# Performance work log

Measured on AMD Instinct MI355X. Metric: run time of the kernel, lower is better.

## Reference

```python
import jax, jax.numpy as jnp
import numpy as np
from jax import lax

B, T, E, H = 256, 512, 256, 256

def setup_inputs() -> dict:
    key = jax.random.key(0)
    k1, k2, k3, k4, k5 = jax.random.split(key, 5)
    s_in = 1.0 / np.sqrt(E)
    s_h = 1.0 / np.sqrt(H)
    return {
        "x": jax.random.normal(k1, (B, T, E), dtype=jnp.float32),
        "Wx_w": jax.random.normal(k2, (H, E), dtype=jnp.float32) * s_in,
        "Wx_b": jax.random.normal(k3, (H,), dtype=jnp.float32) * s_in,
        "Wh_w": jax.random.normal(k4, (H, H), dtype=jnp.float32) * s_h,
        "Wh_b": jax.random.normal(k5, (H,), dtype=jnp.float32) * s_h,
    }

def reference(x, Wx_w, Wx_b, Wh_w, Wh_b):
    # Precompute input gates for all timesteps: g = sigmoid(Wx(x))  [B,T,H]
    gates = jax.nn.sigmoid(jnp.einsum("bte,he->bth", x, Wx_w) + Wx_b)
    h0 = jnp.zeros((x.shape[0], Wh_w.shape[0]), dtype=x.dtype)

    def step(h, g_t):  # g_t: [B,H]
        h_new = h * g_t + (1.0 - g_t) * jnp.tanh(h @ Wh_w.T + Wh_b)
        return h_new, h_new

    _, outs = lax.scan(step, h0, jnp.swapaxes(gates, 0, 1))  # [T,B,H]
    return jnp.swapaxes(outs, 0, 1)  # [B,T,H]
```

## Files before the change

kernel.cpp:

```cpp
#include <hip/hip_runtime.h>

#define Tsz 512
#define Hsz 256

typedef __attribute__((ext_vector_type(8))) short short8;
typedef __attribute__((ext_vector_type(4))) short short4v;
typedef __attribute__((ext_vector_type(4))) float f32x4;

static __device__ __forceinline__ unsigned short f2bf(float f) {
    union { float f; unsigned int i; } v; v.f = f;
    unsigned int r = v.i + 0x7fffu + ((v.i >> 16) & 1u);
    return (unsigned short)(r >> 16);
}
static __device__ __forceinline__ float bf2f(unsigned short u) {
    union { unsigned int i; float f; } v; v.i = ((unsigned int)u) << 16; return v.f;
}
static __device__ __forceinline__ short8 ld8f(const float* p) {
    const float4* q = (const float4*)p;
    float4 a = q[0], b = q[1];
    short8 v;
    v[0] = (short)f2bf(a.x); v[1] = (short)f2bf(a.y); v[2] = (short)f2bf(a.z); v[3] = (short)f2bf(a.w);
    v[4] = (short)f2bf(b.x); v[5] = (short)f2bf(b.y); v[6] = (short)f2bf(b.z); v[7] = (short)f2bf(b.w);
    return v;
}
static __device__ __forceinline__ float sigm(float z) {
    return __builtin_amdgcn_rcpf(1.f + __expf(-z));
}

__global__ __launch_bounds__(256) void cvt_wx(const float* __restrict__ Wxw,
                                              unsigned short* __restrict__ wxbf)
{
    int i = (blockIdx.x * 256 + threadIdx.x) * 4;
    float4 v = *(const float4*)(Wxw + i);
    short4v s4;
    s4[0] = (short)f2bf(v.x); s4[1] = (short)f2bf(v.y);
    s4[2] = (short)f2bf(v.z); s4[3] = (short)f2bf(v.w);
    *(short4v*)(wxbf + i) = s4;
}

#define XP 264
__global__ __launch_bounds__(512, 2) void mgu_fused(
    const float* __restrict__ x,   const unsigned short* __restrict__ wxbf,
    const float* __restrict__ Wxb, const float* __restrict__ Whw,
    const float* __restrict__ Whb, float* __restrict__ out)
{
    __shared__ __align__(16) unsigned short xs[2][16 * XP];
    __shared__ __align__(16) unsigned short gsb[2][16 * 256];
    __shared__ __align__(16) unsigned short hbuf[2][256];

    const int tid  = threadIdx.x;
    const int b    = blockIdx.x;
    const int l    = tid & 63;
    const int w    = tid >> 6;
    const int lo16 = l & 15;
    const int hi   = l >> 4;
    const int n_ep = w * 32 + (hi & 1) * 16 + lo16;

    short8 wfh[2][8];
    float  bh[2], bx[2];
#pragma unroll
    for (int nt = 0; nt < 2; ++nt) {
        int n = w * 32 + nt * 16 + lo16;
        bh[nt] = Whb[n];
        bx[nt] = Wxb[n];
#pragma unroll
        for (int ks = 0; ks < 8; ++ks)
            wfh[nt][ks] = ld8f(Whw + (size_t)n * 256 + ks * 32 + hi * 8);
    }

    const unsigned short* gwb = wxbf + (size_t)(w * 32 + lo16) * 256 + hi * 8;

    const float* xrow = x   + (size_t)b * Tsz * Hsz;
    float*       orow = out + (size_t)b * Tsz * Hsz;

    const int srow = tid >> 6;
    const int sj   = tid & 63;

#pragma unroll
    for (int i = 0; i < 4; ++i) {
        int idx = tid + i * 512;
        int m   = idx >> 6;
        int j   = idx & 63;
        float4 v = *(const float4*)(xrow + (size_t)m * 256 + j * 4);
        short4v s4;
        s4[0] = (short)f2bf(v.x); s4[1] = (short)f2bf(v.y);
        s4[2] = (short)f2bf(v.z); s4[3] = (short)f2bf(v.w);
        *(short4v*)(&xs[m >> 4][(m & 15) * XP + j * 4]) = s4;
    }
    if (tid < 256) hbuf[0][tid] = 0;
    __syncthreads();

    {
        f32x4 ag0 = {0.f, 0.f, 0.f, 0.f}, ag1 = {0.f, 0.f, 0.f, 0.f};
#pragma unroll
        for (int ks = 0; ks < 8; ++ks) {
            short8 afg = *(const short8*)(&xs[0][lo16 * XP + ks * 32 + hi * 8]);
            short8 b0 = *(const short8*)(gwb + ks * 32);
            short8 b1 = *(const short8*)(gwb + 16 * 256 + ks * 32);
            ag0 = __builtin_amdgcn_mfma_f32_16x16x32_bf16(afg, b0, ag0, 0, 0, 0);
            ag1 = __builtin_amdgcn_mfma_f32_16x16x32_bf16(afg, b1, ag1, 0, 0, 0);
        }
#pragma unroll
        for (int r = 0; r < 4; ++r) {
            gsb[0][(hi * 4 + r) * 256 + w * 32 + lo16]      = f2bf(sigm(ag0[r] + bx[0]));
            gsb[0][(hi * 4 + r) * 256 + w * 32 + 16 + lo16] = f2bf(sigm(ag1[r] + bx[1]));
        }
    }

    float  hreg = 0.f;
    float  g_carry = 0.f;
    float4 stg;
    f32x4 accg[2];
    { f32x4 z = {0.f, 0.f, 0.f, 0.f}; accg[0] = z; accg[1] = z; }
    short8 afg;

    for (int c = 0; c < 32; ++c) {
        unsigned short*       xs_rd = xs[(c & 1) ^ 1];
        unsigned short*       xs_wr = xs[c & 1];
        const unsigned short* gs_rd = gsb[c & 1];
        unsigned short*       gs_wr = gsb[(c & 1) ^ 1];
#pragma unroll
        for (int s = 0; s < 16; ++s) {
            const int pp = s & 1;
            const int t  = c * 16 + s;
            __syncthreads();

            float g = (s == 0) ? bf2f(gs_rd[n_ep]) : g_carry;
            if (s < 15) g_carry = bf2f(gs_rd[(s + 1) * 256 + n_ep]);

            short8 gbf = *(const short8*)(gwb + pp * (16 * 256) + (s >> 1) * 32);

            if ((s & 1) == 0)
                afg = *(const short8*)(&xs_rd[lo16 * XP + (s >> 1) * 32 + hi * 8]);

            if (c < 30) {
                if (s == 0)
                    stg = *(const float4*)(xrow + (size_t)((c + 2) * 16 + srow) * 256 + sj * 4);
                if (s == 4) {
                    short4v s4;
                    s4[0] = (short)f2bf(stg.x); s4[1] = (short)f2bf(stg.y);
                    s4[2] = (short)f2bf(stg.z); s4[3] = (short)f2bf(stg.w);
                    *(short4v*)(&xs_wr[srow * XP + sj * 4]) = s4;
                }
                if (s == 8)
                    stg = *(const float4*)(xrow + (size_t)((c + 2) * 16 + 8 + srow) * 256 + sj * 4);
                if (s == 12) {
                    short4v s4;
                    s4[0] = (short)f2bf(stg.x); s4[1] = (short)f2bf(stg.y);
                    s4[2] = (short)f2bf(stg.z); s4[3] = (short)f2bf(stg.w);
                    *(short4v*)(&xs_wr[(8 + srow) * XP + sj * 4]) = s4;
                }
            }

            f32x4 a0lo = {bh[0], 0.f, 0.f, 0.f}, a0hi = {0.f, 0.f, 0.f, 0.f};
            f32x4 a1lo = {bh[1], 0.f, 0.f, 0.f}, a1hi = {0.f, 0.f, 0.f, 0.f};
            {
                short8 afh[4];
#pragma unroll
                for (int ks = 0; ks < 4; ++ks)
                    afh[ks] = *(const short8*)(const void*)(&hbuf[pp][ks * 32 + hi * 8]);
#pragma unroll
                for (int ks = 0; ks < 4; ++ks) {
                    a0lo = __builtin_amdgcn_mfma_f32_16x16x32_bf16(afh[ks], wfh[0][ks], a0lo, 0, 0, 0);
                    a1lo = __builtin_amdgcn_mfma_f32_16x16x32_bf16(afh[ks], wfh[1][ks], a1lo, 0, 0, 0);
                }
            }
            {
                short8 afh[4];
#pragma unroll
                for (int ks = 0; ks < 4; ++ks)
                    afh[ks] = *(const short8*)(const void*)(&hbuf[pp][(ks + 4) * 32 + hi * 8]);
#pragma unroll
                for (int ks = 0; ks < 4; ++ks) {
                    a0hi = __builtin_amdgcn_mfma_f32_16x16x32_bf16(afh[ks], wfh[0][ks + 4], a0hi, 0, 0, 0);
                    a1hi = __builtin_amdgcn_mfma_f32_16x16x32_bf16(afh[ks], wfh[1][ks + 4], a1hi, 0, 0, 0);
                }
            }

            accg[pp] = __builtin_amdgcn_mfma_f32_16x16x32_bf16(afg, gbf, accg[pp], 0, 0, 0);

            float zz = (hi == 0) ? (a0lo[0] + a0hi[0]) : (a1lo[0] + a1hi[0]);
            zz = fminf(fmaxf(zz, -15.f), 15.f);
            float ex = __expf(2.f * zz);
            float th = (ex - 1.f) * __builtin_amdgcn_rcpf(ex + 1.f);
            if (hi < 2) {
                float hn = g * hreg + (1.f - g) * th;
                hreg = hn;
                hbuf[pp ^ 1][n_ep] = f2bf(hn);
                orow[(size_t)t * 256 + n_ep] = hn;
            }

            if (s == 15) {
#pragma unroll
                for (int r = 0; r < 4; ++r) {
                    gs_wr[(hi * 4 + r) * 256 + w * 32 + lo16]      = f2bf(sigm(accg[0][r] + bx[0]));
                    gs_wr[(hi * 4 + r) * 256 + w * 32 + 16 + lo16] = f2bf(sigm(accg[1][r] + bx[1]));
                }
                f32x4 z = {0.f, 0.f, 0.f, 0.f}; accg[0] = z; accg[1] = z;
            }
        }
    }
}

extern "C" void kernel_launch(void* const* d_in, const int* in_sizes, int n_in,
                              void* d_out, int out_size, void* d_ws, size_t ws_size,
                              hipStream_t stream) {
    const float* x   = (const float*)d_in[0];
    const float* Wxw = (const float*)d_in[1];
    const float* Wxb = (const float*)d_in[2];
    const float* Whw = (const float*)d_in[3];
    const float* Whb = (const float*)d_in[4];
    unsigned short* wxbf = (unsigned short*)d_ws;

    cvt_wx<<<dim3(64), dim3(256), 0, stream>>>(Wxw, wxbf);
    mgu_fused<<<dim3(256), dim3(512), 0, stream>>>(x, wxbf, Wxb, Whw, Whb, (float*)d_out);
}
```

Measured before the change: 237.8 us.

## Halve block to four waves, each computing 64 hidden units per step

The recurrence kernel drops from 8 waves of 512 threads to 4 waves of 256 threads. Each wave now owns 64 output columns, holds four Wh tiles in registers and issues twice as many MFMAs per step, and all 64 lanes do useful epilogue work instead of half. The aim is cheaper per-step __syncthreads across fewer waves and less idle-lane waste. In exchange, the serial MFMA chain per wave gets longer and register pressure roughly doubles (wfh grows to 32 short8), which could cause spills.

```diff
diff --git a/kernel.cpp b/kernel.cpp
--- a/kernel.cpp
+++ b/kernel.cpp
@@ -39,7 +39,7 @@
 }
 
 #define XP 264
-__global__ __launch_bounds__(512, 2) void mgu_fused(
+__global__ __launch_bounds__(256, 1) void mgu_fused(
     const float* __restrict__ x,   const unsigned short* __restrict__ wxbf,
     const float* __restrict__ Wxb, const float* __restrict__ Whw,
     const float* __restrict__ Whb, float* __restrict__ out)
@@ -54,31 +54,27 @@
     const int w    = tid >> 6;
     const int lo16 = l & 15;
     const int hi   = l >> 4;
-    const int n_ep = w * 32 + (hi & 1) * 16 + lo16;
-
-    short8 wfh[2][8];
-    float  bh[2], bx[2];
-#pragma unroll
-    for (int nt = 0; nt < 2; ++nt) {
-        int n = w * 32 + nt * 16 + lo16;
-        bh[nt] = Whb[n];
-        bx[nt] = Wxb[n];
+
+    short8 wfh[4][8];
+    float  bh[4], bxv[4];
+#pragma unroll
+    for (int nt = 0; nt < 4; ++nt) {
+        int n = w * 64 + nt * 16 + lo16;
+        bh[nt]  = Whb[n];
+        bxv[nt] = Wxb[n];
 #pragma unroll
         for (int ks = 0; ks < 8; ++ks)
             wfh[nt][ks] = ld8f(Whw + (size_t)n * 256 + ks * 32 + hi * 8);
     }
 
-    const unsigned short* gwb = wxbf + (size_t)(w * 32 + lo16) * 256 + hi * 8;
+    const unsigned short* gwb = wxbf + (size_t)(w * 64 + lo16) * 256 + hi * 8;
 
     const float* xrow = x   + (size_t)b * Tsz * Hsz;
     float*       orow = out + (size_t)b * Tsz * Hsz;
 
-    const int srow = tid >> 6;
-    const int sj   = tid & 63;
-
-#pragma unroll
-    for (int i = 0; i < 4; ++i) {
-        int idx = tid + i * 512;
+#pragma unroll
+    for (int i = 0; i < 8; ++i) {
+        int idx = tid + i * 256;
         int m   = idx >> 6;
         int j   = idx & 63;
         float4 v = *(const float4*)(xrow + (size_t)m * 256 + j * 4);
@@ -87,31 +83,35 @@
         s4[2] = (short)f2bf(v.z); s4[3] = (short)f2bf(v.w);
         *(short4v*)(&xs[m >> 4][(m & 15) * XP + j * 4]) = s4;
     }
-    if (tid < 256) hbuf[0][tid] = 0;
+    hbuf[0][tid] = 0;
     __syncthreads();
 
     {
-        f32x4 ag0 = {0.f, 0.f, 0.f, 0.f}, ag1 = {0.f, 0.f, 0.f, 0.f};
+        f32x4 ag[4];
+#pragma unroll
+        for (int nt = 0; nt < 4; ++nt) { f32x4 z = {0.f, 0.f, 0.f, 0.f}; ag[nt] = z; }
 #pragma unroll
         for (int ks = 0; ks < 8; ++ks) {
-            short8 afg = *(const short8*)(&xs[0][lo16 * XP + ks * 32 + hi * 8]);
-            short8 b0 = *(const short8*)(gwb + ks * 32);
-            short8 b1 = *(const short8*)(gwb + 16 * 256 + ks * 32);
-            ag0 = __builtin_amdgcn_mfma_f32_16x16x32_bf16(afg, b0, ag0, 0, 0, 0);
-            ag1 = __builtin_amdgcn_mfma_f32_16x16x32_bf16(afg, b1, ag1, 0, 0, 0);
+            short8 a = *(const short8*)(&xs[0][lo16 * XP + ks * 32 + hi * 8]);
+#pragma unroll
+            for (int nt = 0; nt < 4; ++nt) {
+                short8 bf = *(const short8*)(gwb + nt * (16 * 256) + ks * 32);
+                ag[nt] = __builtin_amdgcn_mfma_f32_16x16x32_bf16(a, bf, ag[nt], 0, 0, 0);
+            }
         }
 #pragma unroll
-        for (int r = 0; r < 4; ++r) {
-            gsb[0][(hi * 4 + r) * 256 + w * 32 + lo16]      = f2bf(sigm(ag0[r] + bx[0]));
-            gsb[0][(hi * 4 + r) * 256 + w * 32 + 16 + lo16] = f2bf(sigm(ag1[r] + bx[1]));
-        }
+        for (int nt = 0; nt < 4; ++nt)
+#pragma unroll
+            for (int r = 0; r < 4; ++r)
+                gsb[0][(hi * 4 + r) * 256 + w * 64 + nt * 16 + lo16] = f2bf(sigm(ag[nt][r] + bxv[nt]));
     }
 
     float  hreg = 0.f;
     float  g_carry = 0.f;
-    float4 stg;
-    f32x4 accg[2];
-    { f32x4 z = {0.f, 0.f, 0.f, 0.f}; accg[0] = z; accg[1] = z; }
+    float4 stgA, stgB;
+    f32x4 accg[4];
+#pragma unroll
+    for (int nt = 0; nt < 4; ++nt) { f32x4 z = {0.f, 0.f, 0.f, 0.f}; accg[nt] = z; }
     short8 afg;
 
     for (int c = 0; c < 32; ++c) {
@@ -125,78 +125,93 @@
             const int t  = c * 16 + s;
             __syncthreads();
 
-            float g = (s == 0) ? bf2f(gs_rd[n_ep]) : g_carry;
-            if (s < 15) g_carry = bf2f(gs_rd[(s + 1) * 256 + n_ep]);
-
-            short8 gbf = *(const short8*)(gwb + pp * (16 * 256) + (s >> 1) * 32);
+            float g = (s == 0) ? bf2f(gs_rd[tid]) : g_carry;
+            if (s < 15) g_carry = bf2f(gs_rd[(s + 1) * 256 + tid]);
+
+            const int ksg = s >> 1;
+            const int nt0 = (2 * s) & 3, nt1 = (2 * s + 1) & 3;
+            short8 gb0 = *(const short8*)(gwb + nt0 * (16 * 256) + ksg * 32);
+            short8 gb1 = *(const short8*)(gwb + nt1 * (16 * 256) + ksg * 32);
 
             if ((s & 1) == 0)
-                afg = *(const short8*)(&xs_rd[lo16 * XP + (s >> 1) * 32 + hi * 8]);
+                afg = *(const short8*)(&xs_rd[lo16 * XP + ksg * 32 + hi * 8]);
 
             if (c < 30) {
-                if (s == 0)
-                    stg = *(const float4*)(xrow + (size_t)((c + 2) * 16 + srow) * 256 + sj * 4);
+                if (s == 0) {
+                    stgA = *(const float4*)(xrow + (size_t)((c + 2) * 16 + (tid >> 6)) * 256 + (tid & 63) * 4);
+                    stgB = *(const float4*)(xrow + (size_t)((c + 2) * 16 + 4 + (tid >> 6)) * 256 + (tid & 63) * 4);
+                }
                 if (s == 4) {
                     short4v s4;
-                    s4[0] = (short)f2bf(stg.x); s4[1] = (short)f2bf(stg.y);
-                    s4[2] = (short)f2bf(stg.z); s4[3] = (short)f2bf(stg.w);
-                    *(short4v*)(&xs_wr[srow * XP + sj * 4]) = s4;
-                }
-                if (s == 8)
-                    stg = *(const float4*)(xrow + (size_t)((c + 2) * 16 + 8 + srow) * 256 + sj * 4);
+                    s4[0] = (short)f2bf(stgA.x); s4[1] = (short)f2bf(stgA.y);
+                    s4[2] = (short)f2bf(stgA.z); s4[3] = (short)f2bf(stgA.w);
+                    *(short4v*)(&xs_wr[(tid >> 6) * XP + (tid & 63) * 4]) = s4;
+                    s4[0] = (short)f2bf(stgB.x); s4[1] = (short)f2bf(stgB.y);
+                    s4[2] = (short)f2bf(stgB.z); s4[3] = (short)f2bf(stgB.w);
+                    *(short4v*)(&xs_wr[(4 + (tid >> 6)) * XP + (tid & 63) * 4]) = s4;
+                }
+                if (s == 8) {
+                    stgA = *(const float4*)(xrow + (size_t)((c + 2) * 16 + 8 + (tid >> 6)) * 256 + (tid & 63) * 4);
+                    stgB = *(const float4*)(xrow + (size_t)((c + 2) * 16 + 12 + (tid >> 6)) * 256 + (tid & 63) * 4);
+                }
                 if (s == 12) {
                     short4v s4;
-                    s4[0] = (short)f2bf(stg.x); s4[1] = (short)f2bf(stg.y);
-                    s4[2] = (short)f2bf(stg.z); s4[3] = (short)f2bf(stg.w);
-                    *(short4v*)(&xs_wr[(8 + srow) * XP + sj * 4]) = s4;
+                    s4[0] = (short)f2bf(stgA.x); s4[1] = (short)f2bf(stgA.y);
+                    s4[2] = (short)f2bf(stgA.z); s4[3] = (short)f2bf(stgA.w);
+                    *(short4v*)(&xs_wr[(8 + (tid >> 6)) * XP + (tid & 63) * 4]) = s4;
+                    s4[0] = (short)f2bf(stgB.x); s4[1] = (short)f2bf(stgB.y);
+                    s4[2] = (short)f2bf(stgB.z); s4[3] = (short)f2bf(stgB.w);
+                    *(short4v*)(&xs_wr[(12 + (tid >> 6)) * XP + (tid & 63) * 4]) = s4;
                 }
             }
 
             f32x4 a0lo = {bh[0], 0.f, 0.f, 0.f}, a0hi = {0.f, 0.f, 0.f, 0.f};
             f32x4 a1lo = {bh[1], 0.f, 0.f, 0.f}, a1hi = {0.f, 0.f, 0.f, 0.f};
+            f32x4 a2lo = {bh[2], 0.f, 0.f, 0.f}, a2hi = {0.f, 0.f, 0.f, 0.f};
+            f32x4 a3lo = {bh[3], 0.f, 0.f, 0.f}, a3hi = {0.f, 0.f, 0.f, 0.f};
             {
-                short8 afh[4];
+                short8 afhA[4], afhB[4];
 #pragma unroll
                 for (int ks = 0; ks < 4; ++ks)
-                    afh[ks] = *(const short8*)(const void*)(&hbuf[pp][ks * 32 + hi * 8]);
+                    afhA[ks] = *(const short8*)(const void*)(&hbuf[pp][ks * 32 + hi * 8]);
+#pragma unroll
+                for (int ks = 0; ks < 4; ++ks)
+                    afhB[ks] = *(const short8*)(const void*)(&hbuf[pp][(ks + 4) * 32 + hi * 8]);
 #pragma unroll
                 for (int ks = 0; ks < 4; ++ks) {
-                    a0lo = __builtin_amdgcn_mfma_f32_16x16x32_bf16(afh[ks], wfh[0][ks], a0lo, 0, 0, 0);
-                    a1lo = __builtin_amdgcn_mfma_f32_16x16x32_bf16(afh[ks], wfh[1][ks], a1lo, 0, 0, 0);
-                }
-            }
-            {
-                short8 afh[4];
-#pragma unroll
-                for (int ks = 0; ks < 4; ++ks)
-                    afh[ks] = *(const short8*)(const void*)(&hbuf[pp][(ks + 4) * 32 + hi * 8]);
-#pragma unroll
-                for (int ks = 0; ks < 4; ++ks) {
-                    a0hi = __builtin_amdgcn_mfma_f32_16x16x32_bf16(afh[ks], wfh[0][ks + 4], a0hi, 0, 0, 0);
-                    a1hi = __builtin_amdgcn_mfma_f32_16x16x32_bf16(afh[ks], wfh[1][ks + 4], a1hi, 0, 0, 0);
-                }
-            }
-
-            accg[pp] = __builtin_amdgcn_mfma_f32_16x16x32_bf16(afg, gbf, accg[pp], 0, 0, 0);
-
-            float zz = (hi == 0) ? (a0lo[0] + a0hi[0]) : (a1lo[0] + a1hi[0]);
+                    a0lo = __builtin_amdgcn_mfma_f32_16x16x32_bf16(afhA[ks], wfh[0][ks],     a0lo, 0, 0, 0);
+                    a1lo = __builtin_amdgcn_mfma_f32_16x16x32_bf16(afhA[ks], wfh[1][ks],     a1lo, 0, 0, 0);
+                    a2lo = __builtin_amdgcn_mfma_f32_16x16x32_bf16(afhA[ks], wfh[2][ks],     a2lo, 0, 0, 0);
+                    a3lo = __builtin_amdgcn_mfma_f32_16x16x32_bf16(afhA[ks], wfh[3][ks],     a3lo, 0, 0, 0);
+                    a0hi = __builtin_amdgcn_mfma_f32_16x16x32_bf16(afhB[ks], wfh[0][ks + 4], a0hi, 0, 0, 0);
+                    a1hi = __builtin_amdgcn_mfma_f32_16x16x32_bf16(afhB[ks], wfh[1][ks + 4], a1hi, 0, 0, 0);
+                    a2hi = __builtin_amdgcn_mfma_f32_16x16x32_bf16(afhB[ks], wfh[2][ks + 4], a2hi, 0, 0, 0);
+                    a3hi = __builtin_amdgcn_mfma_f32_16x16x32_bf16(afhB[ks], wfh[3][ks + 4], a3hi, 0, 0, 0);
+                }
+            }
+
+            accg[nt0] = __builtin_amdgcn_mfma_f32_16x16x32_bf16(afg, gb0, accg[nt0], 0, 0, 0);
+            accg[nt1] = __builtin_amdgcn_mfma_f32_16x16x32_bf16(afg, gb1, accg[nt1], 0, 0, 0);
+
+            float zz = (hi == 0) ? (a0lo[0] + a0hi[0]) : (hi == 1) ? (a1lo[0] + a1hi[0])
+                     : (hi == 2) ? (a2lo[0] + a2hi[0]) : (a3lo[0] + a3hi[0]);
             zz = fminf(fmaxf(zz, -15.f), 15.f);
             float ex = __expf(2.f * zz);
             float th = (ex - 1.f) * __builtin_amdgcn_rcpf(ex + 1.f);
-            if (hi < 2) {
-                float hn = g * hreg + (1.f - g) * th;
-                hreg = hn;
-                hbuf[pp ^ 1][n_ep] = f2bf(hn);
-                orow[(size_t)t * 256 + n_ep] = hn;
-            }
+            float hn = th + g * (hreg - th);
+            hreg = hn;
+            hbuf[pp ^ 1][tid] = f2bf(hn);
+            orow[(size_t)t * 256 + tid] = hn;
 
             if (s == 15) {
 #pragma unroll
-                for (int r = 0; r < 4; ++r) {
-                    gs_wr[(hi * 4 + r) * 256 + w * 32 + lo16]      = f2bf(sigm(accg[0][r] + bx[0]));
-                    gs_wr[(hi * 4 + r) * 256 + w * 32 + 16 + lo16] = f2bf(sigm(accg[1][r] + bx[1]));
-                }
-                f32x4 z = {0.f, 0.f, 0.f, 0.f}; accg[0] = z; accg[1] = z;
+                for (int nt = 0; nt < 4; ++nt) {
+#pragma unroll
+                    for (int r = 0; r < 4; ++r)
+                        gs_wr[(hi * 4 + r) * 256 + w * 64 + nt * 16 + lo16]
+                            = f2bf(sigm(accg[nt][r] + bxv[nt]));
+                    f32x4 z = {0.f, 0.f, 0.f, 0.f}; accg[nt] = z;
+                }
             }
         }
     }
@@ -213,5 +228,5 @@
     unsigned short* wxbf = (unsigned short*)d_ws;
 
     cvt_wx<<<dim3(64), dim3(256), 0, stream>>>(Wxw, wxbf);
-    mgu_fused<<<dim3(256), dim3(512), 0, stream>>>(x, wxbf, Wxb, Whw, Whb, (float*)d_out);
-}
+    mgu_fused<<<dim3(256), dim3(256), 0, stream>>>(x, wxbf, Wxb, Whw, Whb, (float*)d_out);
+}
```

Measured after the change: 373.2 us. 1.57x slower.

## Rotate per-wave K order and prefetch own h chunk before barrier

Applied to the files above, without the earlier changes.

Each wave now walks the recurrent K dimension in a rotated order starting at its own 32-column chunk. The hidden-state buffer is duplicated so the rotation wraps without index arithmetic. The wave's own chunk is loaded right after it writes it, ahead of the next barrier, since only that wave produces it, so the first MFMA of the next step no longer waits on LDS after the sync. The MFMA chains are interleaved, and the bias add and gate blend are moved off the accumulator init to shorten the per-step serial critical path; this costs a doubled hbuf write and more LDS.

```diff
diff --git a/kernel.cpp b/kernel.cpp
--- a/kernel.cpp
+++ b/kernel.cpp
@@ -46,7 +46,7 @@
 {
     __shared__ __align__(16) unsigned short xs[2][16 * XP];
     __shared__ __align__(16) unsigned short gsb[2][16 * 256];
-    __shared__ __align__(16) unsigned short hbuf[2][256];
+    __shared__ __align__(16) unsigned short hbuf[2][512];
 
     const int tid  = threadIdx.x;
     const int b    = blockIdx.x;
@@ -64,14 +64,20 @@
         bh[nt] = Whb[n];
         bx[nt] = Wxb[n];
 #pragma unroll
-        for (int ks = 0; ks < 8; ++ks)
-            wfh[nt][ks] = ld8f(Whw + (size_t)n * 256 + ks * 32 + hi * 8);
-    }
+        for (int kk = 0; kk < 8; ++kk) {
+            int rks = (w + kk) & 7;
+            wfh[nt][kk] = ld8f(Whw + (size_t)n * 256 + rks * 32 + hi * 8);
+        }
+    }
+    const float bh_ep = (hi == 0) ? bh[0] : bh[1];
 
     const unsigned short* gwb = wxbf + (size_t)(w * 32 + lo16) * 256 + hi * 8;
 
+    const int   hbo = w * 64 + hi * 16;
+    const char* hbb = (const char*)hbuf;
+
     const float* xrow = x   + (size_t)b * Tsz * Hsz;
-    float*       orow = out + (size_t)b * Tsz * Hsz;
+    float*       optr = out + (size_t)b * Tsz * Hsz + n_ep;
 
     const int srow = tid >> 6;
     const int sj   = tid & 63;
@@ -87,8 +93,10 @@
         s4[2] = (short)f2bf(v.z); s4[3] = (short)f2bf(v.w);
         *(short4v*)(&xs[m >> 4][(m & 15) * XP + j * 4]) = s4;
     }
-    if (tid < 256) hbuf[0][tid] = 0;
+    hbuf[0][tid] = 0;
     __syncthreads();
+
+    short8 afh0c = *(const short8*)(hbb + hbo);
 
     {
         f32x4 ag0 = {0.f, 0.f, 0.f, 0.f}, ag1 = {0.f, 0.f, 0.f, 0.f};
@@ -110,8 +118,9 @@
     float  hreg = 0.f;
     float  g_carry = 0.f;
     float4 stg;
+    const f32x4 Z4 = {0.f, 0.f, 0.f, 0.f};
     f32x4 accg[2];
-    { f32x4 z = {0.f, 0.f, 0.f, 0.f}; accg[0] = z; accg[1] = z; }
+    accg[0] = Z4; accg[1] = Z4;
     short8 afg;
 
     for (int c = 0; c < 32; ++c) {
@@ -122,7 +131,6 @@
 #pragma unroll
         for (int s = 0; s < 16; ++s) {
             const int pp = s & 1;
-            const int t  = c * 16 + s;
             __syncthreads();
 
             float g = (s == 0) ? bf2f(gs_rd[n_ep]) : g_carry;
@@ -152,43 +160,49 @@
                 }
             }
 
-            f32x4 a0lo = {bh[0], 0.f, 0.f, 0.f}, a0hi = {0.f, 0.f, 0.f, 0.f};
-            f32x4 a1lo = {bh[1], 0.f, 0.f, 0.f}, a1hi = {0.f, 0.f, 0.f, 0.f};
-            {
-                short8 afh[4];
-#pragma unroll
-                for (int ks = 0; ks < 4; ++ks)
-                    afh[ks] = *(const short8*)(const void*)(&hbuf[pp][ks * 32 + hi * 8]);
-#pragma unroll
-                for (int ks = 0; ks < 4; ++ks) {
-                    a0lo = __builtin_amdgcn_mfma_f32_16x16x32_bf16(afh[ks], wfh[0][ks], a0lo, 0, 0, 0);
-                    a1lo = __builtin_amdgcn_mfma_f32_16x16x32_bf16(afh[ks], wfh[1][ks], a1lo, 0, 0, 0);
-                }
-            }
-            {
-                short8 afh[4];
-#pragma unroll
-                for (int ks = 0; ks < 4; ++ks)
-                    afh[ks] = *(const short8*)(const void*)(&hbuf[pp][(ks + 4) * 32 + hi * 8]);
-#pragma unroll
-                for (int ks = 0; ks < 4; ++ks) {
-                    a0hi = __builtin_amdgcn_mfma_f32_16x16x32_bf16(afh[ks], wfh[0][ks + 4], a0hi, 0, 0, 0);
-                    a1hi = __builtin_amdgcn_mfma_f32_16x16x32_bf16(afh[ks], wfh[1][ks + 4], a1hi, 0, 0, 0);
-                }
-            }
+            const char* hb = hbb + pp * 1024;
+            short8 af1 = *(const short8*)(hb + hbo + 1 * 64);
+            short8 af2 = *(const short8*)(hb + hbo + 2 * 64);
+            short8 af3 = *(const short8*)(hb + hbo + 3 * 64);
+            short8 af4 = *(const short8*)(hb + hbo + 4 * 64);
+            short8 af5 = *(const short8*)(hb + hbo + 5 * 64);
+            short8 af6 = *(const short8*)(hb + hbo + 6 * 64);
+            short8 af7 = *(const short8*)(hb + hbo + 7 * 64);
+
+            f32x4 a0lo = __builtin_amdgcn_mfma_f32_16x16x32_bf16(afh0c, wfh[0][0], Z4, 0, 0, 0);
+            f32x4 a1lo = __builtin_amdgcn_mfma_f32_16x16x32_bf16(afh0c, wfh[1][0], Z4, 0, 0, 0);
+            f32x4 a0hi = __builtin_amdgcn_mfma_f32_16x16x32_bf16(af4,   wfh[0][4], Z4, 0, 0, 0);
+            f32x4 a1hi = __builtin_amdgcn_mfma_f32_16x16x32_bf16(af4,   wfh[1][4], Z4, 0, 0, 0);
+            a0lo = __builtin_amdgcn_mfma_f32_16x16x32_bf16(af1, wfh[0][1], a0lo, 0, 0, 0);
+            a1lo = __builtin_amdgcn_mfma_f32_16x16x32_bf16(af1, wfh[1][1], a1lo, 0, 0, 0);
+            a0hi = __builtin_amdgcn_mfma_f32_16x16x32_bf16(af5, wfh[0][5], a0hi, 0, 0, 0);
+            a1hi = __builtin_amdgcn_mfma_f32_16x16x32_bf16(af5, wfh[1][5], a1hi, 0, 0, 0);
+            a0lo = __builtin_amdgcn_mfma_f32_16x16x32_bf16(af2, wfh[0][2], a0lo, 0, 0, 0);
+            a1lo = __builtin_amdgcn_mfma_f32_16x16x32_bf16(af2, wfh[1][2], a1lo, 0, 0, 0);
+            a0hi = __builtin_amdgcn_mfma_f32_16x16x32_bf16(af6, wfh[0][6], a0hi, 0, 0, 0);
+            a1hi = __builtin_amdgcn_mfma_f32_16x16x32_bf16(af6, wfh[1][6], a1hi, 0, 0, 0);
+            a0lo = __builtin_amdgcn_mfma_f32_16x16x32_bf16(af3, wfh[0][3], a0lo, 0, 0, 0);
+            a1lo = __builtin_amdgcn_mfma_f32_16x16x32_bf16(af3, wfh[1][3], a1lo, 0, 0, 0);
+            a0hi = __builtin_amdgcn_mfma_f32_16x16x32_bf16(af7, wfh[0][7], a0hi, 0, 0, 0);
+            a1hi = __builtin_amdgcn_mfma_f32_16x16x32_bf16(af7, wfh[1][7], a1hi, 0, 0, 0);
 
             accg[pp] = __builtin_amdgcn_mfma_f32_16x16x32_bf16(afg, gbf, accg[pp], 0, 0, 0);
 
-            float zz = (hi == 0) ? (a0lo[0] + a0hi[0]) : (a1lo[0] + a1hi[0]);
+            float zz = ((hi == 0) ? (a0lo[0] + a0hi[0]) : (a1lo[0] + a1hi[0])) + bh_ep;
             zz = fminf(fmaxf(zz, -15.f), 15.f);
             float ex = __expf(2.f * zz);
             float th = (ex - 1.f) * __builtin_amdgcn_rcpf(ex + 1.f);
+            float hn = th + g * (hreg - th);
             if (hi < 2) {
-                float hn = g * hreg + (1.f - g) * th;
                 hreg = hn;
-                hbuf[pp ^ 1][n_ep] = f2bf(hn);
-                orow[(size_t)t * 256 + n_ep] = hn;
+                unsigned short hb16 = f2bf(hn);
+                hbuf[pp ^ 1][n_ep]       = hb16;
+                hbuf[pp ^ 1][n_ep + 256] = hb16;
+                *optr = hn;
             }
+            optr += 256;
+
+            afh0c = *(const short8*)(hbb + (pp ^ 1) * 1024 + hbo);
 
             if (s == 15) {
 #pragma unroll
@@ -196,7 +210,7 @@
                     gs_wr[(hi * 4 + r) * 256 + w * 32 + lo16]      = f2bf(sigm(accg[0][r] + bx[0]));
                     gs_wr[(hi * 4 + r) * 256 + w * 32 + 16 + lo16] = f2bf(sigm(accg[1][r] + bx[1]));
                 }
-                f32x4 z = {0.f, 0.f, 0.f, 0.f}; accg[0] = z; accg[1] = z;
+                accg[0] = Z4; accg[1] = Z4;
             }
         }
     }
```

Measured after the change: 249.5 us. 1.05x slower.
